# Kernel tuning notes

Hardware: AMD Instinct MI355X
Metric: run time of the kernel (lower is better)

Reference implementation:

```python
import jax, jax.numpy as jnp
import numpy as np

N, D, K = 131072, 64, 4096


def setup_inputs() -> dict:
    key = jax.random.key(0)
    k1, k2 = jax.random.split(key)
    x = jax.random.normal(k1, (N, D), dtype=jnp.float32)
    embed = jax.random.normal(k2, (K, D), dtype=jnp.float32)
    return {"x": x, "embed": embed}


def reference(x, embed):
    """EuclideanCodebook forward.

    x:     [N, D] flat input vectors
    embed: [K, D] codebook
    Returns (quantize [N,D], embed_ind [N], cluster_size [K], embed_sum [K,D]).
    cluster_size / embed_sum are the one-hot scatter statistics fed to the
    EMA codebook update (embed_onehot.sum(0) and flatten^T @ embed_onehot).
    """
    num_codes = embed.shape[0]
    x2 = jnp.sum(x * x, axis=-1, keepdims=True)               # [N, 1]
    e2 = jnp.sum(embed * embed, axis=-1)                      # [K]
    dist = x2 - 2.0 * (x @ embed.T) + e2[None, :]             # [N, K]
    embed_ind = jnp.argmin(dist, axis=-1)                     # [N]
    quantize = embed[embed_ind]                               # gather [N, D]
    # scatter statistics for EMA update
    cluster_size = jnp.zeros((num_codes,), x.dtype).at[embed_ind].add(1.0)  # [K]
    embed_sum = jax.ops.segment_sum(x, embed_ind, num_segments=num_codes)   # [K, D]
    return quantize, embed_ind, cluster_size, embed_sum
```

## Files before the change

kernel.cpp:

```cpp
#include <hip/hip_runtime.h>

#define N_ROWS 131072
#define DIM 64
#define K_CODES 4096
#define BROWS 256
#define CK 64
#define NCH (K_CODES / CK)
#define EST 72
#define EPS 0.015625f
#define HEPS 0.0078125f

typedef __attribute__((ext_vector_type(8))) short short8;
typedef __attribute__((ext_vector_type(4))) float f32x4;

__device__ inline unsigned short bf16rn(float f) {
    unsigned int u = __float_as_uint(f);
    u += 0x7FFFu + ((u >> 16) & 1u);
    return (unsigned short)(u >> 16);
}
__device__ inline unsigned int fkey(float f) {
    unsigned int u = __float_as_uint(f);
    return (u & 0x80000000u) ? ~u : (u | 0x80000000u);
}

__global__ void pack_kernel(const float* __restrict__ embed,
                            unsigned short* __restrict__ ebf,
                            float* __restrict__ e2,
                            float* __restrict__ e2h,
                            int* __restrict__ cnt,
                            float* __restrict__ cs) {
    const int g = blockIdx.x * blockDim.x + threadIdx.x;
    for (int i = g; i < K_CODES + K_CODES * DIM; i += K_CODES * 16)
        cs[i] = 0.f;
    if (g == 0) *cnt = 0;

    const int code = g >> 4;
    const int w    = g & 15;
    const int half = w >> 3;
    const int d0   = (w & 7) << 3;
    const float* ep = embed + (size_t)code * DIM + d0;
    float4 f0 = *(const float4*)ep;
    float4 f1 = *(const float4*)(ep + 4);
    float wv[8] = {f0.x, f0.y, f0.z, f0.w, f1.x, f1.y, f1.z, f1.w};
    unsigned short o[8];
    float ssq = 0.f;
#pragma unroll
    for (int j = 0; j < 8; ++j) {
        unsigned short hb = bf16rn(wv[j]);
        if (half == 0) {
            o[j] = hb;
            ssq = fmaf(wv[j], wv[j], ssq);
        } else {
            float hf = __uint_as_float(((unsigned int)hb) << 16);
            o[j] = bf16rn(wv[j] - hf);
        }
    }
    *(uint4*)(ebf + (size_t)code * 128 + half * 64 + d0) = *(uint4*)o;
    ssq += __shfl_xor(ssq, 1, 64);
    ssq += __shfl_xor(ssq, 2, 64);
    ssq += __shfl_xor(ssq, 4, 64);
    if (w == 0) {
        e2[code]  = ssq;
        e2h[code] = -0.5f * ssq;
    }
}

__global__ __launch_bounds__(256, 2) void dist_argmin_kernel(
        const float* __restrict__ x, const unsigned short* __restrict__ ebf,
        const float* __restrict__ e2h, int* __restrict__ ind_ws,
        float* __restrict__ ind_out, int* __restrict__ cnt,
        int* __restrict__ list) {
    __shared__ unsigned short esh[CK * EST];
    __shared__ unsigned short esl[CK * EST];
    __shared__ float e2s[CK];

    const int tid  = threadIdx.x;
    const int l15  = tid & 15;
    const int quad = (tid >> 4) & 3;
    const int wave = tid >> 6;
    const int r0w  = blockIdx.x * BROWS + wave * 64;

    short8 ah[4][2], al[4][2];
#pragma unroll
    for (int i = 0; i < 4; ++i)
#pragma unroll
        for (int s = 0; s < 2; ++s) {
            const float* xp = x + (size_t)(r0w + 16 * i + l15) * DIM + 32 * s + 8 * quad;
            float4 f0 = *(const float4*)xp;
            float4 f1 = *(const float4*)(xp + 4);
            float w[8] = {f0.x, f0.y, f0.z, f0.w, f1.x, f1.y, f1.z, f1.w};
            short8 h, l;
#pragma unroll
            for (int j = 0; j < 8; ++j) {
                unsigned short hb = bf16rn(w[j]);
                float hf = __uint_as_float(((unsigned int)hb) << 16);
                h[j] = (short)hb;
                l[j] = (short)bf16rn(w[j] - hf);
            }
            ah[i][s] = h;
            al[i][s] = l;
        }

    float s1[16], s2[16];
    int c1[16];
#pragma unroll
    for (int t = 0; t < 16; ++t) { s1[t] = -3.4e38f; s2[t] = -3.4e38f; c1[t] = 0; }

    for (int ch = 0; ch < NCH; ++ch) {
        const int c0 = ch * CK;
        __syncthreads();
        {
            const int col = tid >> 2;
            const int dq  = (tid & 3) * 16;
            const unsigned short* pp = ebf + (size_t)(c0 + col) * 128 + dq;
            uint4 h0 = *(const uint4*)pp;
            uint4 h1 = *(const uint4*)(pp + 8);
            uint4 l0 = *(const uint4*)(pp + 64);
            uint4 l1 = *(const uint4*)(pp + 72);
            *(uint4*)(&esh[col * EST + dq])     = h0;
            *(uint4*)(&esh[col * EST + dq + 8]) = h1;
            *(uint4*)(&esl[col * EST + dq])     = l0;
            *(uint4*)(&esl[col * EST + dq + 8]) = l1;
            if (tid < CK) e2s[tid] = e2h[c0 + tid];
        }
        __syncthreads();

        f32x4 acc[4][4];
#pragma unroll
        for (int j = 0; j < 4; ++j) {
            const float ev = e2s[16 * j + l15];
            const f32x4 iv = {ev, ev, ev, ev};
#pragma unroll
            for (int i = 0; i < 4; ++i) acc[i][j] = iv;
        }

#pragma unroll
        for (int j = 0; j < 4; ++j) {
            const int cb = (16 * j + l15) * EST + 8 * quad;
            short8 bh0 = *(const short8*)(&esh[cb]);
            short8 bh1 = *(const short8*)(&esh[cb + 32]);
            short8 bl0 = *(const short8*)(&esl[cb]);
            short8 bl1 = *(const short8*)(&esl[cb + 32]);
#pragma unroll
            for (int i = 0; i < 4; ++i) {
                f32x4 a = acc[i][j];
                a = __builtin_amdgcn_mfma_f32_16x16x32_bf16(ah[i][0], bh0, a, 0, 0, 0);
                a = __builtin_amdgcn_mfma_f32_16x16x32_bf16(ah[i][1], bh1, a, 0, 0, 0);
                a = __builtin_amdgcn_mfma_f32_16x16x32_bf16(ah[i][0], bl0, a, 0, 0, 0);
                a = __builtin_amdgcn_mfma_f32_16x16x32_bf16(ah[i][1], bl1, a, 0, 0, 0);
                a = __builtin_amdgcn_mfma_f32_16x16x32_bf16(al[i][0], bh0, a, 0, 0, 0);
                a = __builtin_amdgcn_mfma_f32_16x16x32_bf16(al[i][1], bh1, a, 0, 0, 0);
                acc[i][j] = a;
            }
        }

#pragma unroll
        for (int j = 0; j < 4; ++j) {
            const int c = c0 + 16 * j + l15;
#pragma unroll
            for (int i = 0; i < 4; ++i)
#pragma unroll
                for (int r = 0; r < 4; ++r) {
                    float d = acc[i][j][r];
                    const int st = i * 4 + r;
                    bool gt = d > s1[st];
                    s2[st] = fmaxf(fminf(d, s1[st]), s2[st]);
                    c1[st] = gt ? c : c1[st];
                    s1[st] = fmaxf(s1[st], d);
                }
        }
    }

#pragma unroll
    for (int st = 0; st < 16; ++st) {
#pragma unroll
        for (int m = 1; m < 16; m <<= 1) {
            float os1 = __shfl_xor(s1[st], m, 64);
            float os2 = __shfl_xor(s2[st], m, 64);
            int   oc1 = __shfl_xor(c1[st], m, 64);
            bool take = (os1 > s1[st]) || (os1 == s1[st] && oc1 < c1[st]);
            float loser = take ? s1[st] : os1;
            s2[st] = fmaxf(fmaxf(s2[st], os2), loser);
            if (take) { s1[st] = os1; c1[st] = oc1; }
        }
    }
    if (l15 == 0) {
#pragma unroll
        for (int st = 0; st < 16; ++st) {
            const int i = st >> 2, r = st & 3;
            const int row = r0w + 16 * i + 4 * quad + r;
            ind_ws[row] = c1[st];
            ind_out[row] = (float)c1[st];
            if (s1[st] - s2[st] < HEPS) {
                int p = atomicAdd(cnt, 1);
                list[p] = row;
            }
        }
    }
}

__global__ void refine_kernel(const float* __restrict__ x,
                              const float* __restrict__ embed,
                              const float* __restrict__ e2g,
                              const int* __restrict__ cnt,
                              const int* __restrict__ list,
                              int* __restrict__ ind_ws,
                              float* __restrict__ ind_out) {
    __shared__ float xr[DIM];
    __shared__ unsigned long long red[256];
    const int tid = threadIdx.x;
    const int n = *cnt;
    for (int f = blockIdx.x; f < n; f += gridDim.x) {
        const int row = list[f];
        __syncthreads();
        if (tid < 16)
            ((float4*)xr)[tid] = ((const float4*)(x + (size_t)row * DIM))[tid];
        __syncthreads();
        unsigned long long best = ~0ull;
        for (int c = tid; c < K_CODES; c += 256) {
            const float4* ep = (const float4*)(embed + (size_t)c * DIM);
            float d0 = 0.f, d1 = 0.f, d2 = 0.f, d3 = 0.f;
#pragma unroll
            for (int q = 0; q < 16; ++q) {
                float4 ev = ep[q];
                d0 = fmaf(xr[4 * q + 0], ev.x, d0);
                d1 = fmaf(xr[4 * q + 1], ev.y, d1);
                d2 = fmaf(xr[4 * q + 2], ev.z, d2);
                d3 = fmaf(xr[4 * q + 3], ev.w, d3);
            }
            float sc = fmaf(-2.f, (d0 + d1) + (d2 + d3), e2g[c]);
            unsigned long long key =
                ((unsigned long long)fkey(sc) << 32) | (unsigned int)c;
            if (key < best) best = key;
        }
        red[tid] = best;
        __syncthreads();
        for (int w = 128; w > 0; w >>= 1) {
            if (tid < w && red[tid + w] < red[tid]) red[tid] = red[tid + w];
            __syncthreads();
        }
        if (tid == 0) {
            int k = (int)(red[0] & 0xFFFFFFFFull);
            ind_ws[row] = k;
            ind_out[row] = (float)k;
        }
    }
}

__global__ void scatter_kernel(const float* __restrict__ x,
                               const float* __restrict__ embed,
                               const int* __restrict__ ind,
                               float* __restrict__ quant,
                               float* __restrict__ cs,
                               float* __restrict__ esum) {
    const int t = blockIdx.x * blockDim.x + threadIdx.x;
    const int row = t >> 6;
    const int d = t & 63;
    const int k = ind[row];
    quant[t] = embed[(size_t)k * DIM + d];
    atomicAdd(&esum[(size_t)k * DIM + d], x[t]);
    if (d == 0) atomicAdd(&cs[k], 1.0f);
}

extern "C" void kernel_launch(void* const* d_in, const int* in_sizes, int n_in,
                              void* d_out, int out_size, void* d_ws, size_t ws_size,
                              hipStream_t stream) {
    const float* x     = (const float*)d_in[0];
    const float* embed = (const float*)d_in[1];

    float* out     = (float*)d_out;
    float* quant   = out;
    float* ind_out = out + (size_t)N_ROWS * DIM;
    float* cs      = ind_out + N_ROWS;
    float* esum    = cs + K_CODES;

    float* e2   = (float*)d_ws;
    int* cnt    = (int*)(e2 + K_CODES);
    int* list   = cnt + 4;
    int* ind_ws = list + N_ROWS;
    float* e2h  = (float*)(ind_ws + N_ROWS);

    unsigned short* ebf = (unsigned short*)quant;

    pack_kernel<<<(K_CODES * 16) / 256, 256, 0, stream>>>(
        embed, ebf, e2, e2h, cnt, cs);
    dist_argmin_kernel<<<N_ROWS / BROWS, 256, 0, stream>>>(
        x, ebf, e2h, ind_ws, ind_out, cnt, list);
    refine_kernel<<<512, 256, 0, stream>>>(x, embed, e2, cnt, list, ind_ws, ind_out);
    scatter_kernel<<<(size_t)N_ROWS * DIM / 256, 256, 0, stream>>>(
        x, embed, ind_ws, quant, cs, esum);
}
```

Measured before the change: 443.3 us.

## Double-buffer codebook chunks in LDS with register prefetch of next chunk

The codebook chunk staging moves to two LDS buffers. The next chunk's bf16 hi/lo data and e2 values are loaded into registers before the MFMA and argmin work on the current chunk, then written to the alternate buffer afterward. This cuts the two barriers per chunk to one and hides global load latency behind compute. In exchange it doubles LDS use (about 37 KB per block), which may affect the two-blocks-per-CU occupancy target, and it adds register pressure from the prefetch registers.

```diff
diff --git a/kernel.cpp b/kernel.cpp
--- a/kernel.cpp
+++ b/kernel.cpp
@@ -70,15 +70,29 @@
         const float* __restrict__ e2h, int* __restrict__ ind_ws,
         float* __restrict__ ind_out, int* __restrict__ cnt,
         int* __restrict__ list) {
-    __shared__ unsigned short esh[CK * EST];
-    __shared__ unsigned short esl[CK * EST];
-    __shared__ float e2s[CK];
+    __shared__ unsigned short esh[2][CK * EST];
+    __shared__ unsigned short esl[2][CK * EST];
+    __shared__ float e2s[2][CK];
 
     const int tid  = threadIdx.x;
     const int l15  = tid & 15;
     const int quad = (tid >> 4) & 3;
     const int wave = tid >> 6;
     const int r0w  = blockIdx.x * BROWS + wave * 64;
+
+    const int col = tid >> 2;
+    const int dq  = (tid & 3) * 16;
+
+    uint4 sh0, sh1, sl0, sl1;
+    float se2 = 0.f;
+    {
+        const unsigned short* pp = ebf + (size_t)col * 128 + dq;
+        sh0 = *(const uint4*)pp;
+        sh1 = *(const uint4*)(pp + 8);
+        sl0 = *(const uint4*)(pp + 64);
+        sl1 = *(const uint4*)(pp + 72);
+        if (tid < CK) se2 = e2h[tid];
+    }
 
     short8 ah[4][2], al[4][2];
 #pragma unroll
@@ -101,34 +115,37 @@
             al[i][s] = l;
         }
 
+    *(uint4*)(&esh[0][col * EST + dq])     = sh0;
+    *(uint4*)(&esh[0][col * EST + dq + 8]) = sh1;
+    *(uint4*)(&esl[0][col * EST + dq])     = sl0;
+    *(uint4*)(&esl[0][col * EST + dq + 8]) = sl1;
+    if (tid < CK) e2s[0][tid] = se2;
+
     float s1[16], s2[16];
     int c1[16];
 #pragma unroll
     for (int t = 0; t < 16; ++t) { s1[t] = -3.4e38f; s2[t] = -3.4e38f; c1[t] = 0; }
 
+    __syncthreads();
+
+    int cur = 0;
     for (int ch = 0; ch < NCH; ++ch) {
+        {
+            const int c0n = ((ch + 1) & (NCH - 1)) * CK;
+            const unsigned short* pp = ebf + (size_t)(c0n + col) * 128 + dq;
+            sh0 = *(const uint4*)pp;
+            sh1 = *(const uint4*)(pp + 8);
+            sl0 = *(const uint4*)(pp + 64);
+            sl1 = *(const uint4*)(pp + 72);
+            if (tid < CK) se2 = e2h[c0n + tid];
+        }
+
         const int c0 = ch * CK;
-        __syncthreads();
-        {
-            const int col = tid >> 2;
-            const int dq  = (tid & 3) * 16;
-            const unsigned short* pp = ebf + (size_t)(c0 + col) * 128 + dq;
-            uint4 h0 = *(const uint4*)pp;
-            uint4 h1 = *(const uint4*)(pp + 8);
-            uint4 l0 = *(const uint4*)(pp + 64);
-            uint4 l1 = *(const uint4*)(pp + 72);
-            *(uint4*)(&esh[col * EST + dq])     = h0;
-            *(uint4*)(&esh[col * EST + dq + 8]) = h1;
-            *(uint4*)(&esl[col * EST + dq])     = l0;
-            *(uint4*)(&esl[col * EST + dq + 8]) = l1;
-            if (tid < CK) e2s[tid] = e2h[c0 + tid];
-        }
-        __syncthreads();
 
         f32x4 acc[4][4];
 #pragma unroll
         for (int j = 0; j < 4; ++j) {
-            const float ev = e2s[16 * j + l15];
+            const float ev = e2s[cur][16 * j + l15];
             const f32x4 iv = {ev, ev, ev, ev};
 #pragma unroll
             for (int i = 0; i < 4; ++i) acc[i][j] = iv;
@@ -137,10 +154,10 @@
 #pragma unroll
         for (int j = 0; j < 4; ++j) {
             const int cb = (16 * j + l15) * EST + 8 * quad;
-            short8 bh0 = *(const short8*)(&esh[cb]);
-            short8 bh1 = *(const short8*)(&esh[cb + 32]);
-            short8 bl0 = *(const short8*)(&esl[cb]);
-            short8 bl1 = *(const short8*)(&esl[cb + 32]);
+            short8 bh0 = *(const short8*)(&esh[cur][cb]);
+            short8 bh1 = *(const short8*)(&esh[cur][cb + 32]);
+            short8 bl0 = *(const short8*)(&esl[cur][cb]);
+            short8 bl1 = *(const short8*)(&esl[cur][cb + 32]);
 #pragma unroll
             for (int i = 0; i < 4; ++i) {
                 f32x4 a = acc[i][j];
@@ -169,6 +186,16 @@
                     s1[st] = fmaxf(s1[st], d);
                 }
         }
+
+        const int nxt = cur ^ 1;
+        *(uint4*)(&esh[nxt][col * EST + dq])     = sh0;
+        *(uint4*)(&esh[nxt][col * EST + dq + 8]) = sh1;
+        *(uint4*)(&esl[nxt][col * EST + dq])     = sl0;
+        *(uint4*)(&esl[nxt][col * EST + dq + 8]) = sl1;
+        if (tid < CK) e2s[nxt][tid] = se2;
+
+        __syncthreads();
+        cur = nxt;
     }
 
 #pragma unroll
```

New measurement: 436.8 us. No clear change (-1.5%).
